# Optimization experiments

Hardware: AMD Instinct MI355X
Metric: run time of the kernel (lower is better)

## Reference

```python
import jax, jax.numpy as jnp
import numpy as np

B, T, V = 128, 400, 148
E, ENC, DEC, NM, A, H = 512, 512, 1024, 80, 128, 256

def conv1d(x, w, pad):
    # x: [B,C_in,L], w: [C_out,C_in,K]
    return jax.lax.conv_general_dilated(x, w, (1,), [(pad, pad)],
                                        dimension_numbers=('NCH', 'OIH', 'NCH'))

def setup_inputs() -> dict:
    key = jax.random.key(0)
    ks = jax.random.split(key, 40)
    rn = lambda k, shp, s: jax.random.normal(k, shp, jnp.float32) * s
    inp = {
        'text': jax.random.randint(ks[0], (B, T), 0, V, jnp.int32),
        'mels': rn(ks[1], (B, NM, T), 1.0),
        'emb': rn(ks[2], (V, E), 0.3),
        'enc_conv_w': rn(ks[3], (ENC, E, 5), 0.02), 'enc_conv_b': jnp.zeros((ENC,)),
        'bn_g': jnp.ones((ENC,)), 'bn_b': jnp.zeros((ENC,)),
        'lstm_Wih': rn(ks[4], (3, 2, 4 * H, ENC), 0.04),
        'lstm_Whh': rn(ks[5], (3, 2, 4 * H, H), 0.06),
        'lstm_b': jnp.zeros((3, 2, 4 * H)),
        'pre_W1': rn(ks[6], (256, NM), 0.1), 'pre_b1': jnp.zeros((256,)),
        'pre_W2': rn(ks[7], (256, 256), 0.06), 'pre_b2': jnp.zeros((256,)),
        'att_Wq': rn(ks[8], (A, DEC), 0.03), 'att_Wm': rn(ks[9], (A, ENC), 0.04),
        'att_Wloc': rn(ks[10], (A, 2, 31), 0.1), 'att_v': rn(ks[11], (A,), 1.0),
        'dec_Wih': rn(ks[12], (4 * DEC, 256 + ENC), 0.03),
        'dec_Whh': rn(ks[13], (4 * DEC, DEC), 0.03),
        'dec_b': jnp.zeros((4 * DEC,)),
        'out_W': rn(ks[14], (NM * 3, DEC + ENC), 0.025), 'out_b': jnp.zeros((NM * 3,)),
        'post_w1': rn(ks[15], (512, NM, 5), 0.05), 'post_b1': jnp.zeros((512,)),
        'post_g': jnp.ones((512,)), 'post_bta': jnp.zeros((512,)),
        'post_w2': rn(ks[16], (NM, 512, 5), 0.02), 'post_b2': jnp.zeros((NM,)),
    }
    return inp

def reference(text, mels, emb, enc_conv_w, enc_conv_b, bn_g, bn_b,
              lstm_Wih, lstm_Whh, lstm_b, pre_W1, pre_b1, pre_W2, pre_b2,
              att_Wq, att_Wm, att_Wloc, att_v, dec_Wih, dec_Whh, dec_b,
              out_W, out_b, post_w1, post_b1, post_g, post_bta, post_w2, post_b2):
    b, t = text.shape
    n_mels = mels.shape[1]
    # --- encoder ---
    x = emb[text].transpose(0, 2, 1)                        # [B,E,T]
    x = jax.nn.relu(conv1d(x, enc_conv_w, 2) + enc_conv_b[None, :, None])
    mu = x.mean(axis=(0, 2), keepdims=True)
    var = x.var(axis=(0, 2), keepdims=True)                 # BatchNorm1d, train mode
    x = (x - mu) / jnp.sqrt(var + 1e-5) * bn_g[None, :, None] + bn_b[None, :, None]
    h = x.transpose(2, 0, 1)                                # [T,B,ENC] time-major

    def lstm_scan(seq, Wih, Whh, bb, rev):
        def step(carry, xt):
            hh, cc = carry
            g = xt @ Wih.T + hh @ Whh.T + bb
            i, f, gg, o = jnp.split(g, 4, axis=-1)
            cc = jax.nn.sigmoid(f) * cc + jax.nn.sigmoid(i) * jnp.tanh(gg)
            hh = jax.nn.sigmoid(o) * jnp.tanh(cc)
            return (hh, cc), hh
        z = jnp.zeros((seq.shape[1], Whh.shape[-1]), seq.dtype)
        _, hs = jax.lax.scan(step, (z, z), seq, reverse=rev)
        return hs

    for l in range(3):                                      # 3-layer biLSTM
        fwd = lstm_scan(h, lstm_Wih[l, 0], lstm_Whh[l, 0], lstm_b[l, 0], False)
        bwd = lstm_scan(h, lstm_Wih[l, 1], lstm_Whh[l, 1], lstm_b[l, 1], True)
        h = jnp.concatenate([fwd, bwd], axis=-1)            # [T,B,ENC]
    memory = h.transpose(1, 0, 2)                           # [B,T,ENC]
    pm = memory @ att_Wm.T                                  # [B,T,A] (constant over steps)
    mels_tm = mels.transpose(2, 0, 1)                       # [T,B,NM] teacher forcing
    D = dec_Whh.shape[-1]

    def dec_step(carry, mel_t):
        dec_in, hd, cd, cum = carry                         # cum: [B,2,T]
        pre = jax.nn.relu(jax.nn.relu(dec_in @ pre_W1.T + pre_b1) @ pre_W2.T + pre_b2)
        pl = conv1d(cum, att_Wloc, 15)                      # [B,A,T]
        pq = hd @ att_Wq.T                                  # [B,A]
        e = jnp.tanh(pq[:, None, :] + pm + pl.transpose(0, 2, 1)) @ att_v  # [B,T]
        align = jax.nn.softmax(e, axis=-1)
        ctx = jnp.einsum('bt,btd->bd', align, memory)       # [B,ENC]
        cum = cum + align[:, None, :]
        g = jnp.concatenate([pre, ctx], -1) @ dec_Wih.T + hd @ dec_Whh.T + dec_b
        i, f, gg, o = jnp.split(g, 4, axis=-1)
        cd = jax.nn.sigmoid(f) * cd + jax.nn.sigmoid(i) * jnp.tanh(gg)
        hd = jax.nn.sigmoid(o) * jnp.tanh(cd)
        mo = (jnp.concatenate([hd, ctx], -1) @ out_W.T + out_b).reshape(-1, 3, n_mels)
        gate = jax.nn.sigmoid(mo[:, :, -1])                 # [B,3]
        return (mel_t, hd, cd, cum), (mo, gate)

    dt = mels.dtype
    carry0 = (jnp.zeros((b, n_mels), dt), jnp.zeros((b, D), dt),
              jnp.zeros((b, D), dt), jnp.zeros((b, 2, t), dt))
    _, (mos, gates) = jax.lax.scan(dec_step, carry0, mels_tm)
    mel_outputs = mos.transpose(1, 0, 2, 3).reshape(b, 3 * t, n_mels).transpose(0, 2, 1)  # [B,NM,3T]
    gate_outputs = gates.transpose(1, 0, 2).reshape(b, 3 * t)
    # --- postnet ---
    p = conv1d(mel_outputs, post_w1, 2) + post_b1[None, :, None]
    mu = p.mean(axis=(0, 2), keepdims=True)
    var = p.var(axis=(0, 2), keepdims=True)
    p = (p - mu) / jnp.sqrt(var + 1e-5) * post_g[None, :, None] + post_bta[None, :, None]
    p = conv1d(jnp.tanh(p), post_w2, 2) + post_b2[None, :, None]
    mel_postnet = p + mel_outputs
    return mel_outputs, mel_postnet, gate_outputs
```

## Files before the change

### kernel.cpp

```cpp
#include <hip/hip_runtime.h>
#include <hip/hip_fp16.h>
#include <cstdio>
#include <cstddef>

typedef unsigned short u16;
typedef unsigned int u32;

#define BB   128
#define TT   400
#define EE   512
#define HH   256
#define NMEL 80
#define AA   128
#define DD   1024
#define T3   1200
#define PRESPLIT 352

__device__ __forceinline__ float b2f(u16 h) { return __uint_as_float(((u32)h) << 16); }
__device__ __forceinline__ u16 f2b(float f) {
    u32 x = __float_as_uint(f);
    u32 r = (x + 0x7FFFu + ((x >> 16) & 1u)) >> 16;
    return (u16)r;
}
__device__ __forceinline__ float sigm(float x) { return 1.0f / (1.0f + __expf(-x)); }

template<int F32> __device__ __forceinline__ float ldf(const void* p, size_t i) {
    if (F32) return ((const float*)p)[i];
    return b2f(((const u16*)p)[i]);
}
template<int F32> __device__ __forceinline__ float4 ldf4(const void* p, size_t i) {
    if (F32) return *(const float4*)((const float*)p + i);
    ushort4 w = *(const ushort4*)((const u16*)p + i);
    return make_float4(b2f(w.x), b2f(w.y), b2f(w.z), b2f(w.w));
}
template<int F32> __device__ __forceinline__ void stf(void* p, size_t i, float v) {
    if (F32) ((float*)p)[i] = v;
    else ((u16*)p)[i] = f2b(v);
}

__global__ __launch_bounds__(256) void k_detect(const void* emb, int* flag) {
    int tid = threadIdx.x;
    const u16* p = (const u16*)emb;
    int insane = 0;
    for (int i = tid; i < 4096; i += 256) {
        u16 h = p[2 * i];
        u32 ex = (h >> 7) & 0xFF;
        if (ex < 96 || ex > 159) insane++;
    }
    __shared__ int red[256];
    red[tid] = insane; __syncthreads();
    for (int st = 128; st > 0; st >>= 1) {
        if (tid < st) red[tid] += red[tid + st];
        __syncthreads();
    }
    if (tid == 0) *flag = (red[0] > 1024) ? 1 : 0;
}

template<int F32> __device__ __forceinline__ void embed_body(const int* text, const void* emb, float* X) {
    int e = blockIdx.x, b = blockIdx.y;
    for (int t = threadIdx.x; t < TT; t += 256) {
        int v = text[b * TT + t];
        X[((size_t)b * EE + e) * TT + t] = ldf<F32>(emb, (size_t)v * EE + e);
    }
}
__global__ __launch_bounds__(256) void k_embed(const int* text, const void* emb, float* X, const int* flag) {
    if (*flag) embed_body<1>(text, emb, X); else embed_body<0>(text, emb, X);
}

template<int F32> __device__ __forceinline__
void encconv_body(const float* X, const void* W, const void* bias, float* Y, float* xs) {
    int t0 = blockIdx.x * 64, o0 = blockIdx.y * 32, b = blockIdx.z;
    int tid = threadIdx.x;
    int ol = tid >> 3, tg = tid & 7;
    int o = o0 + ol, tl = tg * 8;
    float acc[8];
    float bv = ldf<F32>(bias, o);
    #pragma unroll
    for (int j = 0; j < 8; ++j) acc[j] = bv;
    for (int q = 0; q < 4; ++q) {
        __syncthreads();
        for (int idx = tid; idx < 128 * 68; idx += 256) {
            int il = idx / 68, rest = idx - il * 68;
            int t = t0 - 2 + rest;
            float v = 0.f;
            if (t >= 0 && t < TT) v = X[((size_t)b * EE + q * 128 + il) * TT + t];
            xs[idx] = v;
        }
        __syncthreads();
        size_t wbase = ((size_t)o * EE + q * 128) * 5;
        for (int il = 0; il < 128; ++il) {
            float xv[12];
            #pragma unroll
            for (int j = 0; j < 12; ++j) xv[j] = xs[il * 68 + tl + j];
            #pragma unroll
            for (int k = 0; k < 5; ++k) {
                float w = ldf<F32>(W, wbase + il * 5 + k);
                #pragma unroll
                for (int j = 0; j < 8; ++j) acc[j] += w * xv[j + k];
            }
        }
    }
    #pragma unroll
    for (int j = 0; j < 8; ++j) {
        int t = t0 + tl + j;
        if (t < TT) Y[((size_t)b * EE + o) * TT + t] = acc[j] > 0.f ? acc[j] : 0.f;
    }
}
__global__ __launch_bounds__(256) void k_encconv(const float* X, const void* W, const void* bias, float* Y, const int* flag) {
    __shared__ float xs[128 * 68];
    if (*flag) encconv_body<1>(X, W, bias, Y, xs); else encconv_body<0>(X, W, bias, Y, xs);
}

template<int INF32> __device__ __forceinline__
void bnstats_body(const void* Y, float* mu, float* rs, int L, int C, int Bn) {
    int o = blockIdx.x, tid = threadIdx.x;
    float s = 0.f, s2 = 0.f;
    for (int b = 0; b < Bn; ++b) {
        size_t base = ((size_t)b * C + o) * L;
        for (int t = tid; t < L; t += 256) {
            float v = INF32 ? ((const float*)Y)[base + t] : b2f(((const u16*)Y)[base + t]);
            s += v; s2 += v * v;
        }
    }
    __shared__ float r1[256], r2[256];
    r1[tid] = s; r2[tid] = s2; __syncthreads();
    for (int st = 128; st > 0; st >>= 1) {
        if (tid < st) { r1[tid] += r1[tid + st]; r2[tid] += r2[tid + st]; }
        __syncthreads();
    }
    if (tid == 0) {
        float n = (float)Bn * (float)L;
        float m = r1[0] / n;
        float var = r2[0] / n - m * m;
        mu[o] = m;
        rs[o] = 1.0f / sqrtf(var + 1e-5f);
    }
}
__global__ __launch_bounds__(256) void k_bnstats(const void* Y, float* mu, float* rs, int L, int C, int Bn, int inf32) {
    if (inf32) bnstats_body<1>(Y, mu, rs, L, C, Bn); else bnstats_body<0>(Y, mu, rs, L, C, Bn);
}

template<int F32> __device__ __forceinline__
void bnapply_body(const float* Y, const float* mu, const float* rs, const void* g, const void* beta,
                  float* H, float* tile) {
    int t0 = blockIdx.x * 64, c0 = blockIdx.y * 64, b = blockIdx.z;
    int tid = threadIdx.x;
    for (int idx = tid; idx < 64 * 64; idx += 256) {
        int cl = idx >> 6, tl = idx & 63;
        int t = t0 + tl, c = c0 + cl;
        float v = 0.f;
        if (t < TT) v = Y[((size_t)b * EE + c) * TT + t];
        tile[cl * 65 + tl] = (v - mu[c]) * rs[c] * ldf<F32>(g, c) + ldf<F32>(beta, c);
    }
    __syncthreads();
    for (int idx = tid; idx < 64 * 64; idx += 256) {
        int tl = idx >> 6, cl = idx & 63;
        int t = t0 + tl;
        if (t < TT) H[((size_t)t * BB + b) * EE + c0 + cl] = tile[cl * 65 + tl];
    }
}
__global__ __launch_bounds__(256) void k_bnapply(const float* Y, const float* mu, const float* rs,
                                                 const void* g, const void* beta, float* H, const int* flag) {
    __shared__ float tile[64 * 65];
    if (*flag) bnapply_body<1>(Y, mu, rs, g, beta, H, tile); else bnapply_body<0>(Y, mu, rs, g, beta, H, tile);
}

template<int F32> __device__ __forceinline__
void transEnc_body(const void* Wih, const void* Whh, float* WtE) {
    int ld = blockIdx.x;
    int k  = blockIdx.y;
    int u  = threadIdx.x;
    float4 w;
    if (k < 512) {
        size_t base = (size_t)ld * 1024 * 512;
        w.x = ldf<F32>(Wih, base + (size_t)(u)       * 512 + k);
        w.y = ldf<F32>(Wih, base + (size_t)(256 + u) * 512 + k);
        w.z = ldf<F32>(Wih, base + (size_t)(512 + u) * 512 + k);
        w.w = ldf<F32>(Wih, base + (size_t)(768 + u) * 512 + k);
    } else {
        size_t base = (size_t)ld * 1024 * 256;
        int kk = k - 512;
        w.x = ldf<F32>(Whh, base + (size_t)(u)       * 256 + kk);
        w.y = ldf<F32>(Whh, base + (size_t)(256 + u) * 256 + kk);
        w.z = ldf<F32>(Whh, base + (size_t)(512 + u) * 256 + kk);
        w.w = ldf<F32>(Whh, base + (size_t)(768 + u) * 256 + kk);
    }
    ((float4*)WtE)[((size_t)ld * 768 + k) * 256 + u] = w;
}
__global__ __launch_bounds__(256) void k_transEnc(const void* Wih, const void* Whh, float* WtE, const int* flag) {
    if (*flag) transEnc_body<1>(Wih, Whh, WtE); else transEnc_body<0>(Wih, Whh, WtE);
}

template<int F32> __device__ __forceinline__
void lstm2_body(const float* Hin, float* Hout, const float* WtE, const void* b_all, int layer,
                float* xsh, float* hsh) {
    int d = blockIdx.x >> 6;
    int b0 = (blockIdx.x & 63) * 2;
    int u = threadIdx.x;
    int ld = layer * 2 + d;
    size_t bB = (size_t)ld * 1024;
    float bi_ = ldf<F32>(b_all, bB + u),       bf_ = ldf<F32>(b_all, bB + 256 + u);
    float bg_ = ldf<F32>(b_all, bB + 512 + u), bo_ = ldf<F32>(b_all, bB + 768 + u);
    const float4* W4 = (const float4*)WtE + (size_t)ld * 768 * 256 + u;
    float c0v = 0.f, c1v = 0.f;
    hsh[u] = 0.f; hsh[256 + u] = 0.f;
    for (int s = 0; s < TT; ++s) {
        int t = d ? (TT - 1 - s) : s;
        __syncthreads();
        const float* src = Hin + ((size_t)t * BB + b0) * EE;
        xsh[u] = src[u];             xsh[256 + u] = src[256 + u];
        xsh[512 + u] = src[512 + u]; xsh[768 + u] = src[768 + u];
        __syncthreads();
        float a0i = bi_, a0f = bf_, a0g = bg_, a0o = bo_;
        float a1i = bi_, a1f = bf_, a1g = bg_, a1o = bo_;
        #pragma unroll 8
        for (int k = 0; k < 512; ++k) {
            float4 w = W4[(size_t)k * 256];
            float x0 = xsh[k], x1 = xsh[512 + k];
            a0i += w.x * x0; a0f += w.y * x0; a0g += w.z * x0; a0o += w.w * x0;
            a1i += w.x * x1; a1f += w.y * x1; a1g += w.z * x1; a1o += w.w * x1;
        }
        #pragma unroll 8
        for (int k = 0; k < 256; ++k) {
            float4 w = W4[(size_t)(512 + k) * 256];
            float h0 = hsh[k], h1 = hsh[256 + k];
            a0i += w.x * h0; a0f += w.y * h0; a0g += w.z * h0; a0o += w.w * h0;
            a1i += w.x * h1; a1f += w.y * h1; a1g += w.z * h1; a1o += w.w * h1;
        }
        float i0 = sigm(a0i), f0 = sigm(a0f), g0 = tanhf(a0g), o0v = sigm(a0o);
        c0v = f0 * c0v + i0 * g0;
        float h0v = o0v * tanhf(c0v);
        float i1 = sigm(a1i), f1 = sigm(a1f), g1 = tanhf(a1g), o1v = sigm(a1o);
        c1v = f1 * c1v + i1 * g1;
        float h1v = o1v * tanhf(c1v);
        __syncthreads();
        hsh[u] = h0v; hsh[256 + u] = h1v;
        Hout[((size_t)t * BB + b0) * EE + d * HH + u]     = h0v;
        Hout[((size_t)t * BB + b0 + 1) * EE + d * HH + u] = h1v;
    }
}
__global__ __launch_bounds__(256) void k_lstm2(const float* Hin, float* Hout, const float* WtE,
                                               const void* bb, int layer, const int* flag) {
    __shared__ __align__(16) float xsh[1024];
    __shared__ __align__(16) float hsh[512];
    if (*flag) lstm2_body<1>(Hin, Hout, WtE, bb, layer, xsh, hsh);
    else       lstm2_body<0>(Hin, Hout, WtE, bb, layer, xsh, hsh);
}

template<int F32> __device__ __forceinline__
void pm_body(const float* H1, const void* Wm, float* PM, float* xsh) {
    int t0 = blockIdx.x * 8, b = blockIdx.y;
    int tid = threadIdx.x;
    for (int idx = tid; idx < 8 * 512; idx += 128) {
        int tt = idx >> 9, k = idx & 511;
        xsh[tt * 512 + k] = H1[((size_t)(t0 + tt) * BB + b) * EE + k];
    }
    __syncthreads();
    size_t wrow = (size_t)tid * 512;
    float acc[8] = {0, 0, 0, 0, 0, 0, 0, 0};
    for (int k = 0; k < 512; k += 4) {
        float4 w = ldf4<F32>(Wm, wrow + k);
        #pragma unroll
        for (int tt = 0; tt < 8; ++tt) {
            float4 x = *(const float4*)&xsh[tt * 512 + k];
            acc[tt] += w.x * x.x; acc[tt] += w.y * x.y; acc[tt] += w.z * x.z; acc[tt] += w.w * x.w;
        }
    }
    #pragma unroll
    for (int tt = 0; tt < 8; ++tt)
        PM[((size_t)(t0 + tt) * BB + b) * AA + tid] = acc[tt];
}
__global__ __launch_bounds__(128) void k_pm(const float* H1, const void* Wm, float* PM, const int* flag) {
    __shared__ __align__(16) float xsh[8 * 512];
    if (*flag) pm_body<1>(H1, Wm, PM, xsh); else pm_body<0>(H1, Wm, PM, xsh);
}

template<int F32> __device__ __forceinline__
void transPre_body(const void* W1, const void* W2, float* W1t, float* W2t) {
    int r = blockIdx.x, j = threadIdx.x;
    if (r < 80) W1t[r * 256 + j] = ldf<F32>(W1, (size_t)j * 80 + r);
    else { int k = r - 80; W2t[k * 256 + j] = ldf<F32>(W2, (size_t)j * 256 + k); }
}
__global__ __launch_bounds__(256) void k_transPre(const void* W1, const void* W2, float* W1t, float* W2t, const int* flag) {
    if (*flag) transPre_body<1>(W1, W2, W1t, W2t); else transPre_body<0>(W1, W2, W1t, W2t);
}

template<int F32> __device__ __forceinline__
void prenet_all_body(const void* mels, const float* W1t, const float* W2t, const void* b1, const void* b2,
                     float* PREm, float* PREt, float* melsh, float* h1sh) {
    int t0 = blockIdx.x * 16, b = blockIdx.y;
    int tid = threadIdx.x;
    for (int idx = tid; idx < 16 * 80; idx += 256) {
        int tl = idx / 80, m = idx - tl * 80;
        int t = t0 + tl;
        melsh[tl * 80 + m] = (t == 0) ? 0.f : ldf<F32>(mels, ((size_t)b * NMEL + m) * TT + (t - 1));
    }
    __syncthreads();
    {
        int j = tid;
        float acc[16];
        float bv = ldf<F32>(b1, j);
        #pragma unroll
        for (int tl = 0; tl < 16; ++tl) acc[tl] = bv;
        for (int m = 0; m < 80; ++m) {
            float w = W1t[m * 256 + j];
            #pragma unroll
            for (int tl = 0; tl < 16; ++tl) acc[tl] += w * melsh[tl * 80 + m];
        }
        #pragma unroll
        for (int tl = 0; tl < 16; ++tl) h1sh[tl * 256 + j] = acc[tl] > 0.f ? acc[tl] : 0.f;
    }
    __syncthreads();
    {
        int j = tid;
        float acc[16];
        float bv = ldf<F32>(b2, j);
        #pragma unroll
        for (int tl = 0; tl < 16; ++tl) acc[tl] = bv;
        for (int k = 0; k < 256; ++k) {
            float w = W2t[k * 256 + j];
            #pragma unroll
            for (int tl = 0; tl < 16; ++tl) acc[tl] += w * h1sh[tl * 256 + k];
        }
        #pragma unroll
        for (int tl = 0; tl < 16; ++tl) {
            float v = acc[tl] > 0.f ? acc[tl] : 0.f;
            size_t ix = ((size_t)(t0 + tl) * BB + b) * HH + j;
            if (t0 < PRESPLIT) PREm[ix] = v;
            else               PREt[ix - (size_t)PRESPLIT * BB * HH] = v;
        }
    }
}
__global__ __launch_bounds__(256) void k_prenet_all(const void* mels, const float* W1t, const float* W2t,
                                                    const void* b1, const void* b2,
                                                    float* PREm, float* PREt, const int* flag) {
    __shared__ float melsh[16 * 80];
    __shared__ float h1sh[16 * 256];
    if (*flag) prenet_all_body<1>(mels, W1t, W2t, b1, b2, PREm, PREt, melsh, h1sh);
    else       prenet_all_body<0>(mels, W1t, W2t, b1, b2, PREm, PREt, melsh, h1sh);
}

__global__ void k_weff(const void* Wloc, float* weff, const int* flag) {
    int a = threadIdx.x;
    if (*flag) {
        for (int k = 0; k < 31; ++k)
            weff[a * 31 + k] = ldf<1>(Wloc, (size_t)(a * 2) * 31 + k) + ldf<1>(Wloc, (size_t)(a * 2 + 1) * 31 + k);
    } else {
        for (int k = 0; k < 31; ++k)
            weff[a * 31 + k] = ldf<0>(Wloc, (size_t)(a * 2) * 31 + k) + ldf<0>(Wloc, (size_t)(a * 2 + 1) * 31 + k);
    }
}

template<int F32> __device__ __forceinline__
void transW_body(const void* Wih, const void* Whh, float* Wt2) {
    int u = blockIdx.x * 256 + threadIdx.x;
    int k = blockIdx.y;
    float4 w;
    if (k < 768) {
        w.x = ldf<F32>(Wih, (size_t)(0 * 1024 + u) * 768 + k);
        w.y = ldf<F32>(Wih, (size_t)(1 * 1024 + u) * 768 + k);
        w.z = ldf<F32>(Wih, (size_t)(2 * 1024 + u) * 768 + k);
        w.w = ldf<F32>(Wih, (size_t)(3 * 1024 + u) * 768 + k);
    } else {
        int kk = k - 768;
        w.x = ldf<F32>(Whh, (size_t)(0 * 1024 + u) * 1024 + kk);
        w.y = ldf<F32>(Whh, (size_t)(1 * 1024 + u) * 1024 + kk);
        w.z = ldf<F32>(Whh, (size_t)(2 * 1024 + u) * 1024 + kk);
        w.w = ldf<F32>(Whh, (size_t)(3 * 1024 + u) * 1024 + kk);
    }
    ((float4*)Wt2)[(size_t)k * 1024 + u] = w;
}
__global__ __launch_bounds__(256) void k_transW(const void* Wih, const void* Whh, float* Wt2, const int* flag) {
    if (*flag) transW_body<1>(Wih, Whh, Wt2); else transW_body<0>(Wih, Whh, Wt2);
}

__global__ __launch_bounds__(256) void k_transOut(const void* outW, float* outWt, const int* flag) {
    int k = blockIdx.x;
    int j = threadIdx.x;
    if (j < 240) {
        float v = (*flag) ? ldf<1>(outW, (size_t)j * 1536 + k) : ldf<0>(outW, (size_t)j * 1536 + k);
        outWt[(size_t)k * 240 + j] = v;
    }
}
__global__ __launch_bounds__(128) void k_transWq(const void* Wq, float* Wqt, const int* flag) {
    int k = blockIdx.x;
    int a = threadIdx.x;
    float v = (*flag) ? ldf<1>(Wq, (size_t)a * 1024 + k) : ldf<0>(Wq, (size_t)a * 1024 + k);
    Wqt[(size_t)k * AA + a] = v;
}

template<int F32> __device__ __forceinline__
void att_body(const float* hin, const float* ctxp, float* ctxc,
              const float* Wqt, const float* PM, float* cum, const float* weff,
              const void* att_v, const float* outWt, const void* outB, void* dout,
              const float* H1, int t,
              float* xsh, float* opart, float* pqsh, float* cpad, float* al, float* part, float* red)
{
    int b = blockIdx.x, tid = threadIdx.x;
    xsh[tid]       = hin[(size_t)b * DD + tid];
    xsh[512 + tid] = hin[(size_t)b * DD + 512 + tid];
    if (t > 0) xsh[1024 + (tid & 511)] = ctxp[(size_t)b * EE + (tid & 511)];
    for (int i = tid; i < 432; i += 512) {
        int pos = i - 15;
        cpad[i] = (pos >= 0 && pos < TT) ? cum[b * TT + pos] : 0.f;
    }
    __syncthreads();

    if (t > 0) {
        int j = -1, half = 0;
        if (tid < 240) { j = tid; half = 0; }
        else if (tid >= 256 && tid < 496) { j = tid - 256; half = 1; }
        if (j >= 0) {
            const float* wp = outWt + (half ? (size_t)768 * 240 : 0);
            const float* xp = xsh + (half ? 768 : 0);
            float a0 = 0, a1 = 0, a2 = 0, a3 = 0;
            for (int k = 0; k < 768; k += 4) {
                a0 += wp[(size_t)(k + 0) * 240 + j] * xp[k + 0];
                a1 += wp[(size_t)(k + 1) * 240 + j] * xp[k + 1];
                a2 += wp[(size_t)(k + 2) * 240 + j] * xp[k + 2];
                a3 += wp[(size_t)(k + 3) * 240 + j] * xp[k + 3];
            }
            opart[half * 240 + j] = (a0 + a1) + (a2 + a3);
        }
        __syncthreads();
        if (tid < 240) {
            float acc = ldf<F32>(outB, tid) + opart[tid] + opart[240 + tid];
            int jj = tid / 80, mm = tid - jj * 80;
            int col = 3 * (t - 1) + jj;
            stf<F32>(dout, (size_t)b * 96000 + (size_t)mm * 1200 + col, acc);
            if (mm == 79) stf<F32>(dout, (size_t)24576000 + (size_t)b * 1200 + col, sigm(acc));
        }
    }

    {
        int a = tid & 127, q = tid >> 7;
        float acc = 0.f;
        const float* wq = Wqt + a;
        int k0 = q * 256;
        for (int k = k0; k < k0 + 256; k += 4) {
            acc += wq[(size_t)(k + 0) * AA] * xsh[k + 0];
            acc += wq[(size_t)(k + 1) * AA] * xsh[k + 1];
            acc += wq[(size_t)(k + 2) * AA] * xsh[k + 2];
            acc += wq[(size_t)(k + 3) * AA] * xsh[k + 3];
        }
        pqsh[q * 128 + a] = acc;
    }
    __syncthreads();

    {
        int a = tid & 127, q = tid >> 7;
        float pqv = pqsh[a] + pqsh[128 + a] + pqsh[256 + a] + pqsh[384 + a];
        float vv = ldf<F32>(att_v, a);
        float wr[31];
        #pragma unroll
        for (int k = 0; k < 31; ++k) wr[k] = weff[a * 31 + k];
        int lane = tid & 63;
        int wid2 = (tid >> 6) & 1;
        for (int tt = q; tt < TT; tt += 4) {
            float acc = pqv + PM[((size_t)tt * BB + b) * AA + a];
            #pragma unroll
            for (int k = 0; k < 31; ++k) acc += wr[k] * cpad[tt + k];
            float fv = tanhf(acc) * vv;
            #pragma unroll
            for (int m = 1; m < 64; m <<= 1) fv += __shfl_xor(fv, m, 64);
            if (lane == 0) part[tt * 2 + wid2] = fv;
        }
    }
    __syncthreads();

    float mx = -1e30f;
    for (int tt = tid; tt < TT; tt += 512) { float v = part[2 * tt] + part[2 * tt + 1]; al[tt] = v; mx = fmaxf(mx, v); }
    red[tid] = mx; __syncthreads();
    for (int st = 256; st > 0; st >>= 1) { if (tid < st) red[tid] = fmaxf(red[tid], red[tid + st]); __syncthreads(); }
    mx = red[0]; __syncthreads();
    float s = 0.f;
    for (int tt = tid; tt < TT; tt += 512) { float v = __expf(al[tt] - mx); al[tt] = v; s += v; }
    red[tid] = s; __syncthreads();
    for (int st = 256; st > 0; st >>= 1) { if (tid < st) red[tid] += red[tid + st]; __syncthreads(); }
    float inv = 1.0f / red[0];
    __syncthreads();
    for (int tt = tid; tt < TT; tt += 512) { float v = al[tt] * inv; al[tt] = v; cum[b * TT + tt] += v; }
    __syncthreads();

    {
        int d = tid;
        float a0 = 0, a1 = 0, a2 = 0, a3 = 0;
        for (int tt = 0; tt < TT; tt += 4) {
            a0 += al[tt + 0] * H1[((size_t)(tt + 0) * BB + b) * EE + d];
            a1 += al[tt + 1] * H1[((size_t)(tt + 1) * BB + b) * EE + d];
            a2 += al[tt + 2] * H1[((size_t)(tt + 2) * BB + b) * EE + d];
            a3 += al[tt + 3] * H1[((size_t)(tt + 3) * BB + b) * EE + d];
        }
        ctxc[(size_t)b * EE + d] = (a0 + a1) + (a2 + a3);
    }
}
__global__ __launch_bounds__(512) void k_att(const float* hin, const float* ctxp, float* ctxc,
                                             const float* Wqt, const float* PM, float* cum, const float* weff,
                                             const void* att_v, const float* outWt, const void* outB, void* dout,
                                             const float* H1, int t, const int* flag) {
    __shared__ __align__(16) float xsh[1536];
    __shared__ float opart[480];
    __shared__ float pqsh[512];
    __shared__ float cpad[432];
    __shared__ float al[400];
    __shared__ float part[800];
    __shared__ float red[512];
    if (*flag) att_body<1>(hin, ctxp, ctxc, Wqt, PM, cum, weff, att_v, outWt, outB, dout, H1, t,
                           xsh, opart, pqsh, cpad, al, part, red);
    else       att_body<0>(hin, ctxp, ctxc, Wqt, PM, cum, weff, att_v, outWt, outB, dout, H1, t,
                           xsh, opart, pqsh, cpad, al, part, red);
}

__global__ __launch_bounds__(512) void k_dec_lstm2(const float* PREm, const float* PREt,
                                                   const float* ctx, const float* hd_in,
                                                   const float* Wt2, const void* bbp,
                                                   float* hd_out, float* cd, int t, const int* flag) {
    __shared__ float xs[896 * 9];
    int bt = blockIdx.x >> 4, ut = blockIdx.x & 15;
    int b0 = bt * 8, u0 = ut * 64;
    int tid = threadIdx.x;
    int u_l = tid & 63, bq = tid >> 6;
    int u = u0 + u_l, b = b0 + bq;
    int f32 = *flag;
    const float* prep = (t < PRESPLIT) ? (PREm + (size_t)t * BB * HH)
                                       : (PREt + (size_t)(t - PRESPLIT) * BB * HH);
    float ai, af, ag, ao;
    if (f32) {
        ai = ldf<1>(bbp, u);        af = ldf<1>(bbp, u + 1024);
        ag = ldf<1>(bbp, u + 2048); ao = ldf<1>(bbp, u + 3072);
    } else {
        ai = ldf<0>(bbp, u);        af = ldf<0>(bbp, u + 1024);
        ag = ldf<0>(bbp, u + 2048); ao = ldf<0>(bbp, u + 3072);
    }
    for (int ch = 0; ch < 2; ++ch) {
        __syncthreads();
        for (int idx = tid; idx < 896 * 8; idx += 512) {
            int b_l = idx / 896, kl = idx - b_l * 896;
            int k = ch * 896 + kl;
            int bb_ = b0 + b_l;
            float v;
            if (k < 256)      v = prep[(size_t)bb_ * HH + k];
            else if (k < 768) v = ctx[(size_t)bb_ * EE + (k - 256)];
            else              v = hd_in[(size_t)bb_ * DD + (k - 768)];
            xs[kl * 9 + b_l] = v;
        }
        __syncthreads();
        const float4* wp = (const float4*)Wt2 + (size_t)(ch * 896) * 1024 + u;
        #pragma unroll 8
        for (int kl = 0; kl < 896; ++kl) {
            float4 w = wp[(size_t)kl * 1024];
            float x = xs[kl * 9 + bq];
            ai += w.x * x; af += w.y * x; ag += w.z * x; ao += w.w * x;
        }
    }
    float iv = sigm(ai), fv = sigm(af), gv = tanhf(ag), ov = sigm(ao);
    float c = cd[(size_t)b * DD + u];
    c = fv * c + iv * gv;
    cd[(size_t)b * DD + u] = c;
    hd_out[(size_t)b * DD + u] = ov * tanhf(c);
}

template<int F32> __device__ __forceinline__
void dec_out_body(const float* hd, const float* ctx, const float* outWt, const void* outB,
                  void* dout, int t, float* xsh) {
    int b = blockIdx.x, tid = threadIdx.x;
    for (int idx = tid; idx < 1536; idx += 256)
        xsh[idx] = (idx < 1024) ? hd[(size_t)b * DD + idx] : ctx[(size_t)b * EE + (idx - 1024)];
    __syncthreads();
    if (tid < 240) {
        float a0 = 0, a1 = 0, a2 = 0, a3 = 0;
        for (int k = 0; k < 1536; k += 4) {
            a0 += outWt[(size_t)(k + 0) * 240 + tid] * xsh[k + 0];
            a1 += outWt[(size_t)(k + 1) * 240 + tid] * xsh[k + 1];
            a2 += outWt[(size_t)(k + 2) * 240 + tid] * xsh[k + 2];
            a3 += outWt[(size_t)(k + 3) * 240 + tid] * xsh[k + 3];
        }
        float acc = ldf<F32>(outB, tid) + ((a0 + a1) + (a2 + a3));
        int j = tid / 80, mm = tid - j * 80;
        int col = 3 * t + j;
        stf<F32>(dout, (size_t)b * 96000 + (size_t)mm * 1200 + col, acc);
        if (mm == 79) stf<F32>(dout, (size_t)24576000 + (size_t)b * 1200 + col, sigm(acc));
    }
}
__global__ __launch_bounds__(256) void k_dec_out2(const float* hd, const float* ctx, const float* outWt,
                                                  const void* outB, void* dout, int t, const int* flag) {
    __shared__ __align__(16) float xsh[1536];
    if (*flag) dec_out_body<1>(hd, ctx, outWt, outB, dout, t, xsh);
    else       dec_out_body<0>(hd, ctx, outWt, outB, dout, t, xsh);
}

template<int F32> __device__ __forceinline__
void post1_body(const void* dout, const void* W, const void* bias, u16* P1, u16* msh) {
    int t0 = blockIdx.x * 64, o0 = blockIdx.y * 32, b = blockIdx.z;
    int tid = threadIdx.x;
    for (int idx = tid; idx < 80 * 68; idx += 256) {
        int i = idx / 68, rest = idx - i * 68;
        int t = t0 - 2 + rest;
        u16 v = 0;
        if (t >= 0 && t < T3) v = f2b(ldf<F32>(dout, (size_t)b * 96000 + (size_t)i * 1200 + t));
        msh[idx] = v;
    }
    __syncthreads();
    int ol = tid >> 3, tg = tid & 7;
    int o = o0 + ol, tl = tg * 8;
    float acc[8];
    float bv = ldf<F32>(bias, o);
    #pragma unroll
    for (int j = 0; j < 8; ++j) acc[j] = bv;
    size_t wrow = (size_t)o * 400;
    for (int i = 0; i < 80; ++i) {
        float xv[12];
        #pragma unroll
        for (int j = 0; j < 12; ++j) xv[j] = b2f(msh[i * 68 + tl + j]);
        #pragma unroll
        for (int k = 0; k < 5; ++k) {
            float w = ldf<F32>(W, wrow + i * 5 + k);
            #pragma unroll
            for (int j = 0; j < 8; ++j) acc[j] += w * xv[j + k];
        }
    }
    #pragma unroll
    for (int j = 0; j < 8; ++j) {
        int t = t0 + tl + j;
        if (t < T3) P1[((size_t)b * EE + o) * T3 + t] = f2b(acc[j]);
    }
}
__global__ __launch_bounds__(256) void k_post1(const void* dout, const void* W, const void* bias,
                                               u16* P1, const int* flag) {
    __shared__ u16 msh[80 * 68];
    if (*flag) post1_body<1>(dout, W, bias, P1, msh); else post1_body<0>(dout, W, bias, P1, msh);
}

template<int F32> __device__ __forceinline__
void post2_body(const u16* P1, const float* mu, const float* rs, const void* g, const void* beta,
                const void* W2, const void* b2v, void* dout, float* tsh) {
    int t0 = blockIdx.x * 32, b = blockIdx.y;
    int tid = threadIdx.x;
    int tl = tid >> 3, mg = tid & 7;
    float acc[10];
    #pragma unroll
    for (int q = 0; q < 10; ++q) acc[q] = ldf<F32>(b2v, mg + 8 * q);
    for (int oc = 0; oc < 4; ++oc) {
        int o0 = oc * 128;
        __syncthreads();
        for (int idx = tid; idx < 128 * 36; idx += 256) {
            int i = idx / 36, rest = idx - i * 36;
            int t = t0 - 2 + rest;
            float v = 0.f;
            if (t >= 0 && t < T3) {
                int o = o0 + i;
                float raw = b2f(P1[((size_t)b * EE + o) * T3 + t]);
                v = tanhf((raw - mu[o]) * rs[o] * ldf<F32>(g, o) + ldf<F32>(beta, o));
            }
            tsh[i * 37 + rest] = v;
        }
        __syncthreads();
        for (int i = 0; i < 128; ++i) {
            float xv[5];
            #pragma unroll
            for (int k = 0; k < 5; ++k) xv[k] = tsh[i * 37 + tl + k];
            #pragma unroll
            for (int q = 0; q < 10; ++q) {
                int m = mg + 8 * q;
                size_t wp = ((size_t)m * 512 + o0 + i) * 5;
                acc[q] += ldf<F32>(W2, wp + 0) * xv[0];
                acc[q] += ldf<F32>(W2, wp + 1) * xv[1];
                acc[q] += ldf<F32>(W2, wp + 2) * xv[2];
                acc[q] += ldf<F32>(W2, wp + 3) * xv[3];
                acc[q] += ldf<F32>(W2, wp + 4) * xv[4];
            }
        }
    }
    int t = t0 + tl;
    if (t < T3) {
        #pragma unroll
        for (int q = 0; q < 10; ++q) {
            int m = mg + 8 * q;
            size_t idx = (size_t)b * 96000 + (size_t)m * 1200 + t;
            float res = ldf<F32>(dout, idx);
            stf<F32>(dout, (size_t)12288000 + idx, acc[q] + res);
        }
    }
}
__global__ __launch_bounds__(256) void k_post2(const u16* P1, const float* mu, const float* rs,
                                               const void* g, const void* beta, const void* W2,
                                               const void* b2v, void* dout, const int* flag) {
    __shared__ float tsh[128 * 37];
    if (*flag) post2_body<1>(P1, mu, rs, g, beta, W2, b2v, dout, tsh);
    else       post2_body<0>(P1, mu, rs, g, beta, W2, b2v, dout, tsh);
}

extern "C" void kernel_launch(void* const* d_in, const int* in_sizes, int n_in,
                              void* d_out, int out_size, void* d_ws, size_t ws_size,
                              hipStream_t stream) {
    const int*  text       = (const int*)d_in[0];
    const void* mels       = d_in[1];
    const void* emb        = d_in[2];
    const void* enc_conv_w = d_in[3];
    const void* enc_conv_b = d_in[4];
    const void* bn_g       = d_in[5];
    const void* bn_b       = d_in[6];
    const void* lstm_Wih   = d_in[7];
    const void* lstm_Whh   = d_in[8];
    const void* lstm_b     = d_in[9];
    const void* pre_W1     = d_in[10];
    const void* pre_b1     = d_in[11];
    const void* pre_W2     = d_in[12];
    const void* pre_b2     = d_in[13];
    const void* att_Wq     = d_in[14];
    const void* att_Wm     = d_in[15];
    const void* att_Wloc   = d_in[16];
    const void* att_v      = d_in[17];
    const void* dec_Wih    = d_in[18];
    const void* dec_Whh    = d_in[19];
    const void* dec_b      = d_in[20];
    const void* out_W      = d_in[21];
    const void* out_b      = d_in[22];
    const void* post_w1    = d_in[23];
    const void* post_b1    = d_in[24];
    const void* post_g     = d_in[25];
    const void* post_bta   = d_in[26];
    const void* post_w2    = d_in[27];
    const void* post_b2    = d_in[28];

    const size_t WS_NEED = 212049924;
    if (ws_size < WS_NEED) {
        fprintf(stderr, "kernel_launch: ws_size %zu < needed %zu\n", ws_size, WS_NEED);
        return;
    }
    char* ws = (char*)d_ws;
    float* X    = (float*)(ws + 0);
    float* Yf   = (float*)(ws + 104857600);
    float* H0f  = (float*)(ws + 0);
    float* Af   = (float*)(ws + 104857600);
    float* Bf   = (float*)(ws + 0);
    float* H1f  = (float*)(ws + 104857600);
    float* PM    = (float*)(ws + 0);
    float* Wt2   = (float*)(ws + 26214400);
    float* outWt = (float*)(ws + 55574528);
    float* Wqt   = (float*)(ws + 57049088);
    float* W1t   = (float*)(ws + 57573376);
    float* W2t   = (float*)(ws + 57655296);
    float* PREm  = (float*)(ws + 57917440);
    float* PREt  = (float*)d_out + 12288000;
    u16*   P1    = (u16*)(ws + 0);
    float* WtE   = (float*)d_out;
    char* SM = ws + 209715200;
    float* weff  = (float*)(SM + 0);
    float* encmu = (float*)(SM + 16384);
    float* encrs = (float*)(SM + 18432);
    float* pmu   = (float*)(SM + 20480);
    float* prs   = (float*)(SM + 22528);
    float* cum   = (float*)(SM + 24576);
    float* ctx0  = (float*)(SM + 229376);
    float* ctx1  = (float*)(SM + 491520);
    float* hd0   = (float*)(SM + 753664);
    float* hd1   = (float*)(SM + 1277952);
    float* cd    = (float*)(SM + 1802240);
    int*   flag  = (int*)(SM + 2326528);

    k_detect<<<1, 256, 0, stream>>>(emb, flag);
    hipMemsetAsync(SM, 0, 2326528, stream);
    k_weff<<<1, 128, 0, stream>>>(att_Wloc, weff, flag);
    k_transEnc<<<dim3(6, 768), 256, 0, stream>>>(lstm_Wih, lstm_Whh, WtE, flag);

    k_embed<<<dim3(512, 128), 256, 0, stream>>>(text, emb, X, flag);
    k_encconv<<<dim3(7, 16, 128), 256, 0, stream>>>(X, enc_conv_w, enc_conv_b, Yf, flag);
    k_bnstats<<<512, 256, 0, stream>>>(Yf, encmu, encrs, 400, 512, 128, 1);
    k_bnapply<<<dim3(7, 8, 128), 256, 0, stream>>>(Yf, encmu, encrs, bn_g, bn_b, H0f, flag);
    k_lstm2<<<128, 256, 0, stream>>>(H0f, Af, WtE, lstm_b, 0, flag);
    k_lstm2<<<128, 256, 0, stream>>>(Af, Bf, WtE, lstm_b, 1, flag);
    k_lstm2<<<128, 256, 0, stream>>>(Bf, H1f, WtE, lstm_b, 2, flag);

    k_transW<<<dim3(4, 1792), 256, 0, stream>>>(dec_Wih, dec_Whh, Wt2, flag);
    k_transOut<<<1536, 256, 0, stream>>>(out_W, outWt, flag);
    k_transWq<<<1024, 128, 0, stream>>>(att_Wq, Wqt, flag);
    k_transPre<<<336, 256, 0, stream>>>(pre_W1, pre_W2, W1t, W2t, flag);
    k_pm<<<dim3(50, 128), 128, 0, stream>>>(H1f, att_Wm, PM, flag);
    k_prenet_all<<<dim3(25, 128), 256, 0, stream>>>(mels, W1t, W2t, pre_b1, pre_b2, PREm, PREt, flag);

    for (int t = 0; t < TT; ++t) {
        float* hin  = (t & 1) ? hd1 : hd0;
        float* hout = (t & 1) ? hd0 : hd1;
        float* ctxp = (t & 1) ? ctx0 : ctx1;
        float* ctxc = (t & 1) ? ctx1 : ctx0;
        k_att<<<128, 512, 0, stream>>>(hin, ctxp, ctxc, Wqt, PM, cum, weff, att_v,
                                       outWt, out_b, d_out, H1f, t, flag);
        k_dec_lstm2<<<256, 512, 0, stream>>>(PREm, PREt, ctxc, hin, Wt2, dec_b, hout, cd, t, flag);
    }
    k_dec_out2<<<128, 256, 0, stream>>>(hd0, ctx1, outWt, out_b, d_out, TT - 1, flag);

    k_post1<<<dim3(19, 16, 128), 256, 0, stream>>>(d_out, post_w1, post_b1, P1, flag);
    k_bnstats<<<512, 256, 0, stream>>>(P1, pmu, prs, 1200, 512, 128, 0);
    k_post2<<<dim3(38, 128), 256, 0, stream>>>(P1, pmu, prs, post_g, post_bta, post_w2, post_b2, d_out, flag);
}
```

Before: 158.5 ms.

## Overlap decoder recurrent hidden GEMM with attention in a combined kernel

```diff
diff --git a/kernel.cpp b/kernel.cpp
--- a/kernel.cpp
+++ b/kernel.cpp
@@ -390,13 +390,13 @@
 }
 
 template<int F32> __device__ __forceinline__
-void att_body(const float* hin, const float* ctxp, float* ctxc,
+void att_body(int b, const float* hin, const float* ctxp, float* ctxc,
               const float* Wqt, const float* PM, float* cum, const float* weff,
               const void* att_v, const float* outWt, const void* outB, void* dout,
               const float* H1, int t,
               float* xsh, float* opart, float* pqsh, float* cpad, float* al, float* part, float* red)
 {
-    int b = blockIdx.x, tid = threadIdx.x;
+    int tid = threadIdx.x;
     xsh[tid]       = hin[(size_t)b * DD + tid];
     xsh[512 + tid] = hin[(size_t)b * DD + 512 + tid];
     if (t > 0) xsh[1024 + (tid & 511)] = ctxp[(size_t)b * EE + (tid & 511)];
@@ -494,28 +494,59 @@
         ctxc[(size_t)b * EE + d] = (a0 + a1) + (a2 + a3);
     }
 }
-__global__ __launch_bounds__(512) void k_att(const float* hin, const float* ctxp, float* ctxc,
-                                             const float* Wqt, const float* PM, float* cum, const float* weff,
-                                             const void* att_v, const float* outWt, const void* outB, void* dout,
-                                             const float* H1, int t, const int* flag) {
-    __shared__ __align__(16) float xsh[1536];
-    __shared__ float opart[480];
-    __shared__ float pqsh[512];
-    __shared__ float cpad[432];
-    __shared__ float al[400];
-    __shared__ float part[800];
-    __shared__ float red[512];
-    if (*flag) att_body<1>(hin, ctxp, ctxc, Wqt, PM, cum, weff, att_v, outWt, outB, dout, H1, t,
-                           xsh, opart, pqsh, cpad, al, part, red);
-    else       att_body<0>(hin, ctxp, ctxc, Wqt, PM, cum, weff, att_v, outWt, outB, dout, H1, t,
-                           xsh, opart, pqsh, cpad, al, part, red);
-}
-
-__global__ __launch_bounds__(512) void k_dec_lstm2(const float* PREm, const float* PREt,
-                                                   const float* ctx, const float* hd_in,
-                                                   const float* Wt2, const void* bbp,
-                                                   float* hd_out, float* cd, int t, const int* flag) {
-    __shared__ float xs[896 * 9];
+
+__device__ __forceinline__
+void gemm_hd_body(int bid, const float* hin, const float* Wt2, float* gpart, float* xs) {
+    int bt = bid >> 4, ut = bid & 15;
+    int b0 = bt * 8, u0 = ut * 64;
+    int tid = threadIdx.x;
+    int u_l = tid & 63, bq = tid >> 6;
+    int u = u0 + u_l;
+    for (int idx = tid; idx < 1024 * 8; idx += 512) {
+        int b_l = idx >> 10, kl = idx & 1023;
+        xs[kl * 9 + b_l] = hin[(size_t)(b0 + b_l) * DD + kl];
+    }
+    __syncthreads();
+    float ai = 0.f, af = 0.f, ag = 0.f, ao = 0.f;
+    const float4* wp = (const float4*)Wt2 + (size_t)768 * 1024 + u;
+    #pragma unroll 8
+    for (int kl = 0; kl < 1024; ++kl) {
+        float4 w = wp[(size_t)kl * 1024];
+        float x = xs[kl * 9 + bq];
+        ai += w.x * x; af += w.y * x; ag += w.z * x; ao += w.w * x;
+    }
+    ((float4*)gpart)[(size_t)(b0 + bq) * 1024 + u] = make_float4(ai, af, ag, ao);
+}
+
+__global__ __launch_bounds__(512) void k_att_gemm(const float* hin, const float* ctxp, float* ctxc,
+                                                  const float* Wqt, const float* PM, float* cum, const float* weff,
+                                                  const void* att_v, const float* outWt, const void* outB, void* dout,
+                                                  const float* H1, const float* Wt2, float* gpart,
+                                                  int t, const int* flag) {
+    __shared__ __align__(16) float smem[9216];
+    if (blockIdx.x < 128) {
+        int b = blockIdx.x;
+        float* xsh   = smem;
+        float* opart = smem + 1536;
+        float* pqsh  = smem + 2016;
+        float* cpad  = smem + 2528;
+        float* al    = smem + 2960;
+        float* part  = smem + 3360;
+        float* red   = smem + 4160;
+        if (*flag) att_body<1>(b, hin, ctxp, ctxc, Wqt, PM, cum, weff, att_v, outWt, outB, dout, H1, t,
+                               xsh, opart, pqsh, cpad, al, part, red);
+        else       att_body<0>(b, hin, ctxp, ctxc, Wqt, PM, cum, weff, att_v, outWt, outB, dout, H1, t,
+                               xsh, opart, pqsh, cpad, al, part, red);
+    } else {
+        gemm_hd_body(blockIdx.x - 128, hin, Wt2, gpart, smem);
+    }
+}
+
+__global__ __launch_bounds__(512) void k_dec_lstm3(const float* PREm, const float* PREt,
+                                                   const float* ctx, const float* Wt2, const void* bbp,
+                                                   const float* gpart, float* hd_out, float* cd,
+                                                   int t, const int* flag) {
+    __shared__ float xs[768 * 9];
     int bt = blockIdx.x >> 4, ut = blockIdx.x & 15;
     int b0 = bt * 8, u0 = ut * 64;
     int tid = threadIdx.x;
@@ -532,27 +563,22 @@
         ai = ldf<0>(bbp, u);        af = ldf<0>(bbp, u + 1024);
         ag = ldf<0>(bbp, u + 2048); ao = ldf<0>(bbp, u + 3072);
     }
-    for (int ch = 0; ch < 2; ++ch) {
-        __syncthreads();
-        for (int idx = tid; idx < 896 * 8; idx += 512) {
-            int b_l = idx / 896, kl = idx - b_l * 896;
-            int k = ch * 896 + kl;
-            int bb_ = b0 + b_l;
-            float v;
-            if (k < 256)      v = prep[(size_t)bb_ * HH + k];
-            else if (k < 768) v = ctx[(size_t)bb_ * EE + (k - 256)];
-            else              v = hd_in[(size_t)bb_ * DD + (k - 768)];
-            xs[kl * 9 + b_l] = v;
-        }
-        __syncthreads();
-        const float4* wp = (const float4*)Wt2 + (size_t)(ch * 896) * 1024 + u;
-        #pragma unroll 8
-        for (int kl = 0; kl < 896; ++kl) {
-            float4 w = wp[(size_t)kl * 1024];
-            float x = xs[kl * 9 + bq];
-            ai += w.x * x; af += w.y * x; ag += w.z * x; ao += w.w * x;
-        }
-    }
+    for (int idx = tid; idx < 768 * 8; idx += 512) {
+        int b_l = idx / 768, kl = idx - b_l * 768;
+        int bb_ = b0 + b_l;
+        float v = (kl < 256) ? prep[(size_t)bb_ * HH + kl] : ctx[(size_t)bb_ * EE + (kl - 256)];
+        xs[kl * 9 + b_l] = v;
+    }
+    __syncthreads();
+    const float4* wp = (const float4*)Wt2 + u;
+    #pragma unroll 8
+    for (int kl = 0; kl < 768; ++kl) {
+        float4 w = wp[(size_t)kl * 1024];
+        float x = xs[kl * 9 + bq];
+        ai += w.x * x; af += w.y * x; ag += w.z * x; ao += w.w * x;
+    }
+    float4 gp = ((const float4*)gpart)[(size_t)b * 1024 + u];
+    ai += gp.x; af += gp.y; ag += gp.z; ao += gp.w;
     float iv = sigm(ai), fv = sigm(af), gv = tanhf(ag), ov = sigm(ao);
     float c = cd[(size_t)b * DD + u];
     c = fv * c + iv * gv;
@@ -743,6 +769,7 @@
     float* W2t   = (float*)(ws + 57655296);
     float* PREm  = (float*)(ws + 57917440);
     float* PREt  = (float*)d_out + 12288000;
+    float* gpart = (float*)d_out + 14000000;
     u16*   P1    = (u16*)(ws + 0);
     float* WtE   = (float*)d_out;
     char* SM = ws + 209715200;
@@ -784,9 +811,9 @@
         float* hout = (t & 1) ? hd0 : hd1;
         float* ctxp = (t & 1) ? ctx0 : ctx1;
         float* ctxc = (t & 1) ? ctx1 : ctx0;
-        k_att<<<128, 512, 0, stream>>>(hin, ctxp, ctxc, Wqt, PM, cum, weff, att_v,
-                                       outWt, out_b, d_out, H1f, t, flag);
-        k_dec_lstm2<<<256, 512, 0, stream>>>(PREm, PREt, ctxc, hin, Wt2, dec_b, hout, cd, t, flag);
+        k_att_gemm<<<384, 512, 0, stream>>>(hin, ctxp, ctxc, Wqt, PM, cum, weff, att_v,
+                                            outWt, out_b, d_out, H1f, Wt2, gpart, t, flag);
+        k_dec_lstm3<<<256, 512, 0, stream>>>(PREm, PREt, ctxc, Wt2, dec_b, gpart, hout, cd, t, flag);
     }
     k_dec_out2<<<128, 256, 0, stream>>>(hd0, ctx1, outWt, out_b, d_out, TT - 1, flag);
 
```

New measurement: 141.5 ms. 10.7% less time.
